# Optimization experiments

Measured on AMD Instinct MI355X. Metric: run time of the kernel, lower is better.

The kernel has to match this reference:

```python
import jax, jax.numpy as jnp
import numpy as np

NUM_ITER = (15 + 45) // 2  # eval mode: fixed 30 iterations
LIVE_THRESHOLD = 0.1
CELL_CH = 16


def _sobel_kernels(dtype):
    s = jnp.array([[-1.0, 0.0, 1.0], [-2.0, 0.0, 2.0], [-1.0, 0.0, 1.0]], dtype=dtype) / 8.0
    kx = jnp.tile(s[None, None], (CELL_CH, 1, 1, 1))      # [16,1,3,3] depthwise
    ky = jnp.tile(s.T[None, None], (CELL_CH, 1, 1, 1))    # transpose(2,3)
    return kx, ky


def _dwconv(x, k):
    # depthwise 3x3 conv, padding=1, groups=16
    return jax.lax.conv_general_dilated(
        x, k, window_strides=(1, 1), padding=((1, 1), (1, 1)),
        dimension_numbers=("NCHW", "OIHW", "NCHW"), feature_group_count=CELL_CH)


def _life_mask(x):
    # 3x3 maxpool (stride 1, pad 1) on channel 0, then threshold
    m = jax.lax.reduce_window(x[:, :1], -jnp.inf, jax.lax.max,
                              (1, 1, 3, 3), (1, 1, 1, 1),
                              ((0, 0), (0, 0), (1, 1), (1, 1)))
    return m > LIVE_THRESHOLD


def setup_inputs() -> dict:
    key = jax.random.key(0)
    k1, k2, k3 = jax.random.split(key, 3)
    N, C, H, W = 32, 10, 128, 128
    inp = jax.random.uniform(k1, (N, C, H, W), dtype=jnp.float32)
    w1 = jax.random.normal(k2, (48, 48), dtype=jnp.float32) / jnp.sqrt(48.0)
    w2 = jax.random.normal(k3, (16, 48), dtype=jnp.float32) * 0.02
    return {"inp": inp, "w1": w1, "w2": w2}


def reference(inp, w1, w2):
    N, C, H, W = inp.shape
    kx, ky = _sobel_kernels(inp.dtype)
    # initialize 16-channel cell state
    cell = jnp.zeros((N, CELL_CH, H, W), inp.dtype)
    cell = cell.at[:, 1:C + 1].set(inp)
    cell = cell.at[:, 0].set(1.0 - inp[:, 0])

    def step(cell, _):
        pre = _life_mask(cell)
        perception = jnp.concatenate([cell, _dwconv(cell, kx), _dwconv(cell, ky)], axis=1)  # [N,48,H,W]
        h = jax.nn.relu(jnp.einsum('oc,nchw->nohw', w1, perception))
        cur = jnp.einsum('oc,nchw->nohw', w2, h) + cell
        post = _life_mask(cur)
        cell = cur * (pre & post).astype(cur.dtype)
        return cell, None

    cell, _ = jax.lax.scan(step, cell, None, length=NUM_ITER)
    return cell[:, 1:C + 1]
```

## Files before the change

kernel.cpp:

```cpp
#include <hip/hip_runtime.h>
#include <hip/hip_bf16.h>
#include <stdint.h>

#define HH 128
#define WW 128
#define NIMG 32
#define CH 16
#define TILE 16
#define LW 20
#define LA (LW * LW)
#define NUM_ITER 30
#define THR 0.1f
#define HWSZ (HH * WW)

#define PSTR 52
#define CS_BYTES (17 * LA * 4)
#define SMEM_BYTES CS_BYTES

typedef __attribute__((ext_vector_type(8))) short bf16x8;
typedef __attribute__((ext_vector_type(4))) float f32x4;
typedef __attribute__((ext_vector_type(4))) short sh4;

__device__ __forceinline__ unsigned short f2bf(float x) {
    return __builtin_bit_cast(unsigned short, __float2bfloat16(x));
}
__device__ __forceinline__ float bf2f(unsigned short h) {
    union { unsigned u; float f; } v; v.u = ((unsigned)h) << 16; return v.f;
}
__device__ __forceinline__ bf16x8 mk8(sh4 a, sh4 b) {
    bf16x8 r;
    r[0] = a.x; r[1] = a.y; r[2] = a.z; r[3] = a.w;
    r[4] = b.x; r[5] = b.y; r[6] = b.z; r[7] = b.w;
    return r;
}
__device__ __forceinline__ sh4 ld4(const unsigned short* p) {
    return *(const sh4*)p;
}
__device__ __forceinline__ float max9(const float* p, int idx, int stride) {
    float a = fmaxf(fmaxf(p[idx - stride - 1], p[idx - stride]), p[idx - stride + 1]);
    float b = fmaxf(fmaxf(p[idx - 1],          p[idx]),          p[idx + 1]);
    float c = fmaxf(fmaxf(p[idx + stride - 1], p[idx + stride]), p[idx + stride + 1]);
    return fmaxf(fmaxf(a, b), c);
}

__global__ __launch_bounds__(256) void init_kernel(const float* __restrict__ inp,
                                                   float* __restrict__ cell) {
    int i = blockIdx.x * 256 + threadIdx.x;
    if (i >= NIMG * CH * HWSZ) return;
    int hw = i % HWSZ;
    int c  = (i / HWSZ) % CH;
    int n  = i / (CH * HWSZ);
    float v;
    if (c == 0)       v = 1.0f - inp[(n * 10 + 0) * HWSZ + hw];
    else if (c <= 10) v = inp[(n * 10 + (c - 1)) * HWSZ + hw];
    else              v = 0.0f;
    cell[i] = v;
}

__global__ void prepack(const float* __restrict__ w1, const float* __restrict__ w2,
                        unsigned short* __restrict__ w1h, unsigned short* __restrict__ w1l,
                        unsigned short* __restrict__ w2h, unsigned short* __restrict__ w2l) {
    int i = threadIdx.x;
    for (int k = i; k < 48 * 48; k += 256) {
        float f = w1[k];
        unsigned short h = f2bf(f);
        w1h[k] = h;
        w1l[k] = f2bf(f - bf2f(h));
    }
    for (int k = i; k < 16 * 48; k += 256) {
        float f = w2[k];
        unsigned short h = f2bf(f);
        w2h[k] = h;
        w2l[k] = f2bf(f - bf2f(h));
    }
}

__device__ __forceinline__ void perception_at(const float* cs, int base, float* p) {
#pragma unroll
    for (int c = 0; c < CH; ++c) {
        const float* cc = cs + c * LA;
        float c00 = cc[base - LW - 1], c01 = cc[base - LW], c02 = cc[base - LW + 1];
        float c10 = cc[base - 1],      c11 = cc[base],      c12 = cc[base + 1];
        float c20 = cc[base + LW - 1], c21 = cc[base + LW], c22 = cc[base + LW + 1];
        p[c]      = c11;
        p[16 + c] = (c02 - c00 + 2.0f * (c12 - c10) + c22 - c20) * 0.125f;
        p[32 + c] = (c20 - c00 + 2.0f * (c21 - c01) + c22 - c02) * 0.125f;
    }
}

__global__ __launch_bounds__(256, 5) void step_kernel(
    const float* __restrict__ cin, float* __restrict__ cout,
    const uint8_t* __restrict__ pre_in, uint8_t* __restrict__ pre_out,
    const unsigned short* __restrict__ w1h_, const unsigned short* __restrict__ w1l_,
    const unsigned short* __restrict__ w2h_, const unsigned short* __restrict__ w2l_,
    int gate) {

    __shared__ __align__(16) char smem[SMEM_BYTES];
    float* cs = (float*)smem;
    unsigned short* Ph = (unsigned short*)smem;

    const int tid = threadIdx.x;
    const int tx = tid & 15, ty = tid >> 4;
    const int lane = tid & 63;
    const int wv = tid >> 6;
    const int px = lane & 15;
    const int kc = lane >> 4;

    const int wgid = blockIdx.x;
    const int xcd = wgid & 7;
    const int s   = wgid >> 3;
    const int n   = (xcd << 2) + (s >> 6);
    const int t_  = s & 63;
    const int bx = (t_ & 7) * TILE;
    const int by = (t_ >> 3) * TILE;

    const float* cbase = cin + (size_t)n * CH * HWSZ;
    const uint8_t* pbase = pre_in + (size_t)n * HWSZ;

    const int lyA = tid / 20, lxA = tid % 20;
    const int gyA = by + lyA - 2, gxA = bx + lxA - 2;
    const bool okA = ((unsigned)gyA < HH) && ((unsigned)gxA < WW);
    const int offA = gyA * WW + gxA;

    const int rB = tid + 256;
    const int lyB = rB / 20, lxB = rB % 20;
    const int gyB = by + lyB - 2, gxB = bx + lxB - 2;
    const bool okB = ((unsigned)gyB < HH) && ((unsigned)gxB < WW);
    const int offB = gyB * WW + gxB;

    const int j0 = tid;
    const int jy0 = j0 / 18, jx0 = j0 % 18;
    const int gy0 = by + jy0 - 1, gx0 = bx + jx0 - 1;
    const bool ok0 = ((unsigned)gy0 < HH) && ((unsigned)gx0 < WW);
    const int goff0 = gy0 * WW + gx0;
    const int lpos0 = (jy0 + 1) * LW + (jx0 + 1);

    const int j1 = tid + 256;
    const int jy1 = j1 / 18, jx1 = j1 % 18;
    const int gy1 = by + jy1 - 1, gx1 = bx + jx1 - 1;
    const bool ok1 = ((unsigned)gy1 < HH) && ((unsigned)gx1 < WW);
    const int goff1 = gy1 * WW + gx1;
    const int lpos1 = (jy1 + 1) * LW + (jx1 + 1);
    const bool hasB = (tid < 68);

    cs[CH * LA + tid] = okA ? cbase[offA] : 0.0f;
    if (tid < 144) cs[CH * LA + rB] = okB ? cbase[offB] : 0.0f;

    float st0[CH - 1];
    {
        const float* gp = cbase + goff0;
#pragma unroll
        for (int c = 1; c < CH; ++c) st0[c - 1] = ok0 ? gp[c * HWSZ] : 0.0f;
    }
    int pv0 = 1;
    if (gate) pv0 = ok0 ? (int)pbase[goff0] : 0;

    float st1[CH - 1];
    int pv1 = 1;
    if (hasB) {
        const float* gp = cbase + goff1;
#pragma unroll
        for (int c = 1; c < CH; ++c) st1[c - 1] = ok1 ? gp[c * HWSZ] : 0.0f;
        if (gate) pv1 = ok1 ? (int)pbase[goff1] : 0;
    }
    __syncthreads();

    {
        const float* rp = cs + CH * LA;
        float pm = max9(rp, lpos0, LW);
        float g0 = 1.0f;
        if (gate) g0 = (pv0 && pm > THR) ? 1.0f : 0.0f;
        cs[lpos0] = rp[lpos0] * g0;
#pragma unroll
        for (int c = 1; c < CH; ++c) cs[c * LA + lpos0] = st0[c - 1] * g0;
    }
    if (hasB) {
        const float* rp = cs + CH * LA;
        float pm = max9(rp, lpos1, LW);
        float g1 = 1.0f;
        if (gate) g1 = (pv1 && pm > THR) ? 1.0f : 0.0f;
        cs[lpos1] = rp[lpos1] * g1;
#pragma unroll
        for (int c = 1; c < CH; ++c) cs[c * LA + lpos1] = st1[c - 1] * g1;
    }
    __syncthreads();

    const int base = (ty + 2) * LW + (tx + 2);
    {
        float pm = max9(cs, base, LW);
        pre_out[(size_t)n * HWSZ + (size_t)(by + ty) * WW + (bx + tx)] = (pm > THR) ? 1 : 0;
    }

    float p[48];
    perception_at(cs, base, p);

    float res[4][4];
#pragma unroll
    for (int t = 0; t < 4; ++t) {
        const int lp = (4 * wv + t + 2) * LW + (px + 2);
#pragma unroll
        for (int r = 0; r < 4; ++r)
            res[t][r] = cs[(4 * kc + r) * LA + lp];
    }
    __syncthreads();

    {
        unsigned short* hrow = Ph + tid * PSTR;
#pragma unroll
        for (int j = 0; j < 12; ++j) {
            sh4 hv;
            hv.x = (short)f2bf(p[4 * j + 0]);
            hv.y = (short)f2bf(p[4 * j + 1]);
            hv.z = (short)f2bf(p[4 * j + 2]);
            hv.w = (short)f2bf(p[4 * j + 3]);
            *(sh4*)(hrow + 4 * j) = hv;
        }
    }

    const sh4 z4 = (sh4)0;
    const bf16x8 zero8 = mk8(z4, z4);

    f32x4 acc[3][4];
#pragma unroll
    for (int m = 0; m < 3; ++m)
#pragma unroll
        for (int t = 0; t < 4; ++t) acc[m][t] = 0.0f;

#pragma unroll
    for (int m = 0; m < 3; ++m) {
        const unsigned short* ah = w1h_ + (16 * m + px) * 48;
        const unsigned short* al = w1l_ + (16 * m + px) * 48;
        bf16x8 Ah1 = mk8(ld4(ah + 8 * kc), ld4(ah + 8 * kc + 4));
        bf16x8 Ah2 = mk8(ld4(ah + 32 + 8 * kc), ld4(ah + 36 + 8 * kc));
        bf16x8 Al1 = mk8(ld4(al + 8 * kc), ld4(al + 8 * kc + 4));
        bf16x8 Al2 = mk8(ld4(al + 32 + 8 * kc), ld4(al + 36 + 8 * kc));
#pragma unroll
        for (int t = 0; t < 4; ++t) {
            const int pix = 64 * wv + 16 * t + px;
            const unsigned short* bh = Ph + pix * PSTR;
            bf16x8 Bh1 = mk8(ld4(bh + 8 * kc), ld4(bh + 8 * kc + 4));
            bf16x8 Bh2 = (kc < 2) ? mk8(ld4(bh + 32 + 8 * kc), ld4(bh + 36 + 8 * kc)) : zero8;
            f32x4 a = acc[m][t];
            a = __builtin_amdgcn_mfma_f32_16x16x32_bf16(Al1, Bh1, a, 0, 0, 0);
            a = __builtin_amdgcn_mfma_f32_16x16x32_bf16(Al2, Bh2, a, 0, 0, 0);
            a = __builtin_amdgcn_mfma_f32_16x16x32_bf16(Ah1, Bh1, a, 0, 0, 0);
            a = __builtin_amdgcn_mfma_f32_16x16x32_bf16(Ah2, Bh2, a, 0, 0, 0);
            acc[m][t] = a;
        }
    }

#pragma unroll
    for (int t = 0; t < 4; ++t) {
        const int pix = 64 * wv + 16 * t + px;
        unsigned short* hrow = Ph + pix * PSTR;
#pragma unroll
        for (int m = 0; m < 3; ++m) {
            f32x4 a = acc[m][t];
            sh4 hv;
            hv.x = (short)f2bf(fmaxf(a[0], 0.0f));
            hv.y = (short)f2bf(fmaxf(a[1], 0.0f));
            hv.z = (short)f2bf(fmaxf(a[2], 0.0f));
            hv.w = (short)f2bf(fmaxf(a[3], 0.0f));
            *(sh4*)(hrow + 16 * m + 4 * kc) = hv;
        }
    }

    {
        const unsigned short* ah = w2h_ + px * 48;
        const unsigned short* al = w2l_ + px * 48;
        bf16x8 A2h1 = mk8(ld4(ah + 8 * kc), ld4(ah + 8 * kc + 4));
        bf16x8 A2h2 = mk8(ld4(ah + 32 + 8 * kc), ld4(ah + 36 + 8 * kc));
        bf16x8 A2l1 = mk8(ld4(al + 8 * kc), ld4(al + 8 * kc + 4));
        bf16x8 A2l2 = mk8(ld4(al + 32 + 8 * kc), ld4(al + 36 + 8 * kc));

        f32x4 q[4];
#pragma unroll
        for (int t = 0; t < 4; ++t) q[t] = 0.0f;
#pragma unroll
        for (int t = 0; t < 4; ++t) {
            const int pix = 64 * wv + 16 * t + px;
            const unsigned short* bh = Ph + pix * PSTR;
            bf16x8 B1 = mk8(ld4(bh + 8 * kc), ld4(bh + 8 * kc + 4));
            bf16x8 B2 = (kc < 2) ? mk8(ld4(bh + 32 + 8 * kc), ld4(bh + 36 + 8 * kc)) : zero8;
            f32x4 a = q[t];
            a = __builtin_amdgcn_mfma_f32_16x16x32_bf16(A2l1, B1, a, 0, 0, 0);
            a = __builtin_amdgcn_mfma_f32_16x16x32_bf16(A2l2, B2, a, 0, 0, 0);
            a = __builtin_amdgcn_mfma_f32_16x16x32_bf16(A2h1, B1, a, 0, 0, 0);
            a = __builtin_amdgcn_mfma_f32_16x16x32_bf16(A2h2, B2, a, 0, 0, 0);
            q[t] = a;
        }

        float* ob = cout + (size_t)n * CH * HWSZ;
#pragma unroll
        for (int t = 0; t < 4; ++t) {
            const int rowoff = (by + 4 * wv + t) * WW + bx + px;
#pragma unroll
            for (int r = 0; r < 4; ++r)
                ob[(size_t)(4 * kc + r) * HWSZ + rowoff] = q[t][r] + res[t][r];
        }
    }
}

__global__ __launch_bounds__(256) void final_kernel(
    const float* __restrict__ cur, const uint8_t* __restrict__ pre,
    float* __restrict__ out) {
    int i = blockIdx.x * 256 + threadIdx.x;
    if (i >= NIMG * HWSZ) return;
    int x = i % WW, y = (i / WW) % HH, n = i / HWSZ;
    const float* c0 = cur + (size_t)n * CH * HWSZ;
    float pm = -1e30f;
    for (int dy = -1; dy <= 1; ++dy) {
        int yy = y + dy;
        if ((unsigned)yy >= HH) continue;
        for (int dx = -1; dx <= 1; ++dx) {
            int xx = x + dx;
            if ((unsigned)xx >= WW) continue;
            pm = fmaxf(pm, c0[yy * WW + xx]);
        }
    }
    const bool alive = pre[i] && (pm > THR);
    float* ob = out + (size_t)n * 10 * HWSZ + y * WW + x;
#pragma unroll
    for (int k = 1; k <= 10; ++k)
        ob[(k - 1) * HWSZ] = alive ? c0[k * HWSZ + y * WW + x] : 0.0f;
}

extern "C" void kernel_launch(void* const* d_in, const int* in_sizes, int n_in,
                              void* d_out, int out_size, void* d_ws, size_t ws_size,
                              hipStream_t stream) {
    const float* inp = (const float*)d_in[0];
    const float* w1  = (const float*)d_in[1];
    const float* w2  = (const float*)d_in[2];
    float* out = (float*)d_out;

    const size_t SE = (size_t)NIMG * CH * HWSZ;
    float* bufA = (float*)d_ws;
    float* bufB = bufA + SE;
    uint8_t* bitsA = (uint8_t*)(bufB + SE);
    uint8_t* bitsB = bitsA + (size_t)NIMG * HWSZ;
    unsigned short* w1h = (unsigned short*)(bitsB + (size_t)NIMG * HWSZ);
    unsigned short* w1l = w1h + (48 * 48 + 32);
    unsigned short* w2h = w1l + (48 * 48 + 32);
    unsigned short* w2l = w2h + (16 * 48 + 32);

    init_kernel<<<((int)SE + 255) / 256, 256, 0, stream>>>(inp, bufA);
    prepack<<<1, 256, 0, stream>>>(w1, w2, w1h, w1l, w2h, w2l);

    const int nblk = (WW / TILE) * (HH / TILE) * NIMG;
    float* src = bufA;
    float* dst = bufB;
    uint8_t* pin = bitsB;
    uint8_t* pout = bitsA;
    for (int it = 0; it < NUM_ITER; ++it) {
        step_kernel<<<nblk, 256, 0, stream>>>(src, dst, pin, pout,
                                              w1h, w1l, w2h, w2l,
                                              it == 0 ? 0 : 1);
        float* t = src; src = dst; dst = t;
        uint8_t* tb = pin; pin = pout; pout = tb;
    }
    final_kernel<<<(NIMG * HWSZ + 255) / 256, 256, 0, stream>>>(src, pin, out);
}
```

Baseline: 1.005 ms.

## Enlarge step tile to 32x16 with 512 threads and fold init into first step

Each step block now covers a 32x16 tile with 512 threads instead of 16x16 with 256. This lowers the halo overhead per output pixel in the staged cell tile. The separate init kernel is removed: on the first iteration the step kernel reads the raw input directly and builds the 16-channel state on the fly, which saves one full pass over the state tensor. Risks: the launch bound of (512, 6) may force tight register limits and cause spills of the 48-value perception array, and the larger LDS use per block reduces how many blocks fit on a CU.

```diff
diff --git a/kernel.cpp b/kernel.cpp
--- a/kernel.cpp
+++ b/kernel.cpp
@@ -6,16 +6,18 @@
 #define WW 128
 #define NIMG 32
 #define CH 16
-#define TILE 16
-#define LW 20
-#define LA (LW * LW)
+#define TX 32
+#define TY 16
+#define LWX 36
+#define LWY 20
+#define LA (LWX * LWY)
 #define NUM_ITER 30
 #define THR 0.1f
 #define HWSZ (HH * WW)
 
 #define PSTR 52
 #define CS_BYTES (17 * LA * 4)
-#define SMEM_BYTES CS_BYTES
+#define SMEM_BYTES (512 * PSTR * 2)
 
 typedef __attribute__((ext_vector_type(8))) short bf16x8;
 typedef __attribute__((ext_vector_type(4))) float f32x4;
@@ -41,20 +43,6 @@
     float b = fmaxf(fmaxf(p[idx - 1],          p[idx]),          p[idx + 1]);
     float c = fmaxf(fmaxf(p[idx + stride - 1], p[idx + stride]), p[idx + stride + 1]);
     return fmaxf(fmaxf(a, b), c);
-}
-
-__global__ __launch_bounds__(256) void init_kernel(const float* __restrict__ inp,
-                                                   float* __restrict__ cell) {
-    int i = blockIdx.x * 256 + threadIdx.x;
-    if (i >= NIMG * CH * HWSZ) return;
-    int hw = i % HWSZ;
-    int c  = (i / HWSZ) % CH;
-    int n  = i / (CH * HWSZ);
-    float v;
-    if (c == 0)       v = 1.0f - inp[(n * 10 + 0) * HWSZ + hw];
-    else if (c <= 10) v = inp[(n * 10 + (c - 1)) * HWSZ + hw];
-    else              v = 0.0f;
-    cell[i] = v;
 }
 
 __global__ void prepack(const float* __restrict__ w1, const float* __restrict__ w2,
@@ -79,28 +67,29 @@
 #pragma unroll
     for (int c = 0; c < CH; ++c) {
         const float* cc = cs + c * LA;
-        float c00 = cc[base - LW - 1], c01 = cc[base - LW], c02 = cc[base - LW + 1];
-        float c10 = cc[base - 1],      c11 = cc[base],      c12 = cc[base + 1];
-        float c20 = cc[base + LW - 1], c21 = cc[base + LW], c22 = cc[base + LW + 1];
+        float c00 = cc[base - LWX - 1], c01 = cc[base - LWX], c02 = cc[base - LWX + 1];
+        float c10 = cc[base - 1],       c11 = cc[base],       c12 = cc[base + 1];
+        float c20 = cc[base + LWX - 1], c21 = cc[base + LWX], c22 = cc[base + LWX + 1];
         p[c]      = c11;
         p[16 + c] = (c02 - c00 + 2.0f * (c12 - c10) + c22 - c20) * 0.125f;
         p[32 + c] = (c20 - c00 + 2.0f * (c21 - c01) + c22 - c02) * 0.125f;
     }
 }
 
-__global__ __launch_bounds__(256, 5) void step_kernel(
-    const float* __restrict__ cin, float* __restrict__ cout,
+__global__ __launch_bounds__(512, 6) void step_kernel(
+    const float* __restrict__ inp, const float* __restrict__ cin,
+    float* __restrict__ cout,
     const uint8_t* __restrict__ pre_in, uint8_t* __restrict__ pre_out,
     const unsigned short* __restrict__ w1h_, const unsigned short* __restrict__ w1l_,
     const unsigned short* __restrict__ w2h_, const unsigned short* __restrict__ w2l_,
-    int gate) {
+    int gate, int first) {
 
     __shared__ __align__(16) char smem[SMEM_BYTES];
     float* cs = (float*)smem;
     unsigned short* Ph = (unsigned short*)smem;
 
     const int tid = threadIdx.x;
-    const int tx = tid & 15, ty = tid >> 4;
+    const int tx2 = tid & 31, ty2 = tid >> 5;
     const int lane = tid & 63;
     const int wv = tid >> 6;
     const int px = lane & 15;
@@ -109,65 +98,81 @@
     const int wgid = blockIdx.x;
     const int xcd = wgid & 7;
     const int s   = wgid >> 3;
-    const int n   = (xcd << 2) + (s >> 6);
-    const int t_  = s & 63;
-    const int bx = (t_ & 7) * TILE;
-    const int by = (t_ >> 3) * TILE;
+    const int n   = (xcd << 2) + (s >> 5);
+    const int t_  = s & 31;
+    const int bx = (t_ & 3) * TX;
+    const int by = (t_ >> 2) * TY;
 
     const float* cbase = cin + (size_t)n * CH * HWSZ;
+    const float* ibase = inp + (size_t)n * 10 * HWSZ;
     const uint8_t* pbase = pre_in + (size_t)n * HWSZ;
 
-    const int lyA = tid / 20, lxA = tid % 20;
+    const int lyA = tid / 36, lxA = tid % 36;
     const int gyA = by + lyA - 2, gxA = bx + lxA - 2;
     const bool okA = ((unsigned)gyA < HH) && ((unsigned)gxA < WW);
     const int offA = gyA * WW + gxA;
 
-    const int rB = tid + 256;
-    const int lyB = rB / 20, lxB = rB % 20;
+    const int rB = tid + 512;
+    const int lyB = rB / 36, lxB = rB % 36;
     const int gyB = by + lyB - 2, gxB = bx + lxB - 2;
     const bool okB = ((unsigned)gyB < HH) && ((unsigned)gxB < WW);
     const int offB = gyB * WW + gxB;
+    const bool hasA2 = (tid < 208);
 
     const int j0 = tid;
-    const int jy0 = j0 / 18, jx0 = j0 % 18;
+    const int jy0 = j0 / 34, jx0 = j0 % 34;
     const int gy0 = by + jy0 - 1, gx0 = bx + jx0 - 1;
     const bool ok0 = ((unsigned)gy0 < HH) && ((unsigned)gx0 < WW);
     const int goff0 = gy0 * WW + gx0;
-    const int lpos0 = (jy0 + 1) * LW + (jx0 + 1);
-
-    const int j1 = tid + 256;
-    const int jy1 = j1 / 18, jx1 = j1 % 18;
+    const int lpos0 = (jy0 + 1) * LWX + (jx0 + 1);
+
+    const int j1 = tid + 512;
+    const int jy1 = j1 / 34, jx1 = j1 % 34;
     const int gy1 = by + jy1 - 1, gx1 = bx + jx1 - 1;
     const bool ok1 = ((unsigned)gy1 < HH) && ((unsigned)gx1 < WW);
     const int goff1 = gy1 * WW + gx1;
-    const int lpos1 = (jy1 + 1) * LW + (jx1 + 1);
-    const bool hasB = (tid < 68);
-
-    cs[CH * LA + tid] = okA ? cbase[offA] : 0.0f;
-    if (tid < 144) cs[CH * LA + rB] = okB ? cbase[offB] : 0.0f;
+    const int lpos1 = (jy1 + 1) * LWX + (jx1 + 1);
+    const bool hasB = (tid < 100);
+
+    if (first) {
+        cs[CH * LA + tid] = okA ? 1.0f - ibase[offA] : 0.0f;
+        if (hasA2) cs[CH * LA + rB] = okB ? 1.0f - ibase[offB] : 0.0f;
+    } else {
+        cs[CH * LA + tid] = okA ? cbase[offA] : 0.0f;
+        if (hasA2) cs[CH * LA + rB] = okB ? cbase[offB] : 0.0f;
+    }
 
     float st0[CH - 1];
-    {
-        const float* gp = cbase + goff0;
-#pragma unroll
-        for (int c = 1; c < CH; ++c) st0[c - 1] = ok0 ? gp[c * HWSZ] : 0.0f;
-    }
-    int pv0 = 1;
-    if (gate) pv0 = ok0 ? (int)pbase[goff0] : 0;
-
     float st1[CH - 1];
-    int pv1 = 1;
-    if (hasB) {
-        const float* gp = cbase + goff1;
-#pragma unroll
-        for (int c = 1; c < CH; ++c) st1[c - 1] = ok1 ? gp[c * HWSZ] : 0.0f;
-        if (gate) pv1 = ok1 ? (int)pbase[goff1] : 0;
+    int pv0 = 1, pv1 = 1;
+    if (first) {
+#pragma unroll
+        for (int c = 1; c < CH; ++c)
+            st0[c - 1] = (c <= 10 && ok0) ? ibase[(c - 1) * HWSZ + goff0] : 0.0f;
+        if (hasB) {
+#pragma unroll
+            for (int c = 1; c < CH; ++c)
+                st1[c - 1] = (c <= 10 && ok1) ? ibase[(c - 1) * HWSZ + goff1] : 0.0f;
+        }
+    } else {
+        {
+            const float* gp = cbase + goff0;
+#pragma unroll
+            for (int c = 1; c < CH; ++c) st0[c - 1] = ok0 ? gp[c * HWSZ] : 0.0f;
+        }
+        if (gate) pv0 = ok0 ? (int)pbase[goff0] : 0;
+        if (hasB) {
+            const float* gp = cbase + goff1;
+#pragma unroll
+            for (int c = 1; c < CH; ++c) st1[c - 1] = ok1 ? gp[c * HWSZ] : 0.0f;
+            if (gate) pv1 = ok1 ? (int)pbase[goff1] : 0;
+        }
     }
     __syncthreads();
 
     {
         const float* rp = cs + CH * LA;
-        float pm = max9(rp, lpos0, LW);
+        float pm = max9(rp, lpos0, LWX);
         float g0 = 1.0f;
         if (gate) g0 = (pv0 && pm > THR) ? 1.0f : 0.0f;
         cs[lpos0] = rp[lpos0] * g0;
@@ -176,7 +181,7 @@
     }
     if (hasB) {
         const float* rp = cs + CH * LA;
-        float pm = max9(rp, lpos1, LW);
+        float pm = max9(rp, lpos1, LWX);
         float g1 = 1.0f;
         if (gate) g1 = (pv1 && pm > THR) ? 1.0f : 0.0f;
         cs[lpos1] = rp[lpos1] * g1;
@@ -185,10 +190,10 @@
     }
     __syncthreads();
 
-    const int base = (ty + 2) * LW + (tx + 2);
+    const int base = (ty2 + 2) * LWX + (tx2 + 2);
     {
-        float pm = max9(cs, base, LW);
-        pre_out[(size_t)n * HWSZ + (size_t)(by + ty) * WW + (bx + tx)] = (pm > THR) ? 1 : 0;
+        float pm = max9(cs, base, LWX);
+        pre_out[(size_t)n * HWSZ + (size_t)(by + ty2) * WW + (bx + tx2)] = (pm > THR) ? 1 : 0;
     }
 
     float p[48];
@@ -197,7 +202,8 @@
     float res[4][4];
 #pragma unroll
     for (int t = 0; t < 4; ++t) {
-        const int lp = (4 * wv + t + 2) * LW + (px + 2);
+        const int pix = 64 * wv + 16 * t + px;
+        const int lp = ((pix >> 5) + 2) * LWX + ((pix & 31) + 2);
 #pragma unroll
         for (int r = 0; r < 4; ++r)
             res[t][r] = cs[(4 * kc + r) * LA + lp];
@@ -293,7 +299,8 @@
         float* ob = cout + (size_t)n * CH * HWSZ;
 #pragma unroll
         for (int t = 0; t < 4; ++t) {
-            const int rowoff = (by + 4 * wv + t) * WW + bx + px;
+            const int pix = 64 * wv + 16 * t + px;
+            const int rowoff = (by + (pix >> 5)) * WW + bx + (pix & 31);
 #pragma unroll
             for (int r = 0; r < 4; ++r)
                 ob[(size_t)(4 * kc + r) * HWSZ + rowoff] = q[t][r] + res[t][r];
@@ -343,18 +350,17 @@
     unsigned short* w2h = w1l + (48 * 48 + 32);
     unsigned short* w2l = w2h + (16 * 48 + 32);
 
-    init_kernel<<<((int)SE + 255) / 256, 256, 0, stream>>>(inp, bufA);
     prepack<<<1, 256, 0, stream>>>(w1, w2, w1h, w1l, w2h, w2l);
 
-    const int nblk = (WW / TILE) * (HH / TILE) * NIMG;
-    float* src = bufA;
-    float* dst = bufB;
+    const int nblk = NIMG * (HH / TY) * (WW / TX);
+    float* src = bufB;
+    float* dst = bufA;
     uint8_t* pin = bitsB;
     uint8_t* pout = bitsA;
     for (int it = 0; it < NUM_ITER; ++it) {
-        step_kernel<<<nblk, 256, 0, stream>>>(src, dst, pin, pout,
+        step_kernel<<<nblk, 512, 0, stream>>>(inp, src, dst, pin, pout,
                                               w1h, w1l, w2h, w2l,
-                                              it == 0 ? 0 : 1);
+                                              it == 0 ? 0 : 1, it == 0 ? 1 : 0);
         float* t = src; src = dst; dst = t;
         uint8_t* tb = pin; pin = pout; pout = tb;
     }
```

Result: slower. 1.071 ms (+6.6%).
